# Optimization experiments

Measured on AMD Instinct MI355X. Metric: run time of the kernel, lower is better.

The kernel has to match this reference:

```python
import jax, jax.numpy as jnp
import numpy as np

N = 50000      # num nodes
E = 800000     # num edges
F = 128        # num_node_features
H = 4          # num_heads
D = 32         # output_dim (per head); H*D == F -> residual is identity
G = 8          # grid_size
K = 3          # spline order (standard KANLinear default)
NEG_SLOPE = 0.2


def _make_grid(grid_size, k):
    # uniform grid on [-1, 1], extended by k on each side: [G + 2k + 1] points
    h = 2.0 / grid_size
    return jnp.arange(-k, grid_size + k + 1, dtype=jnp.float32) * h - 1.0


def _bsplines(x, grid, k):
    # x: [N, F], grid: [G+2k+1] -> bases: [N, F, G+k] (Cox-de Boor recursion)
    xg = x[..., None]
    b = ((xg >= grid[:-1]) & (xg < grid[1:])).astype(x.dtype)
    for j in range(1, k + 1):
        left = (xg - grid[:-(j + 1)]) / (grid[j:-1] - grid[:-(j + 1)]) * b[..., :-1]
        right = (grid[j + 1:] - xg) / (grid[j + 1:] - grid[1:-j]) * b[..., 1:]
        b = left + right
    return b


def _kan_linear(x, base_w, spline_w, grid, k):
    # efficient-KAN linear, no bias: silu(x) @ Wb^T + Bspline(x) contracted with Ws
    base = jax.nn.silu(x) @ base_w.T                      # [N, O]
    bs = _bsplines(x, grid, k)                            # [N, F, G+K]
    spline = jnp.einsum('nfc,ofc->no', bs, spline_w)      # [N, O]
    return base + spline


def setup_inputs() -> dict:
    key = jax.random.key(0)
    ks = jax.random.split(key, 8)
    O = H * D
    C = G + K
    x = jax.random.normal(ks[0], (N, F), dtype=jnp.float32)
    edge_index = jax.random.randint(ks[1], (2, E), 0, N, dtype=jnp.int64)
    scale = 1.0 / np.sqrt(F)
    base_w_src = jax.random.normal(ks[2], (O, F), dtype=jnp.float32) * scale
    spline_w_src = jax.random.normal(ks[3], (O, F, C), dtype=jnp.float32) * (0.1 * scale)
    base_w_dst = jax.random.normal(ks[4], (O, F), dtype=jnp.float32) * scale
    spline_w_dst = jax.random.normal(ks[5], (O, F, C), dtype=jnp.float32) * (0.1 * scale)
    double_attn = jax.random.normal(ks[6], (1, H, D), dtype=jnp.float32) * (1.0 / np.sqrt(D))
    bias = jnp.zeros((O,), dtype=jnp.float32)
    prelu_a = jnp.asarray(0.25, dtype=jnp.float32)  # nn.PReLU default
    return {"x": x, "edge_index": edge_index,
            "base_w_src": base_w_src, "spline_w_src": spline_w_src,
            "base_w_dst": base_w_dst, "spline_w_dst": spline_w_dst,
            "double_attn": double_attn, "bias": bias, "prelu_a": prelu_a}


def reference(x, edge_index, base_w_src, spline_w_src, base_w_dst, spline_w_dst,
              double_attn, bias, prelu_a):
    grid = _make_grid(G, K)
    src = edge_index[0]
    dst = edge_index[1]
    num_nodes = x.shape[0]
    # projections (dropout is identity in eval mode)
    sp = _kan_linear(x, base_w_src, spline_w_src, grid, K).reshape(num_nodes, H, D)
    dp = _kan_linear(x, base_w_dst, spline_w_dst, grid, K).reshape(num_nodes, H, D)
    # GATv2 edge scores: leakyrelu(gather(src) + gather(dst)), then attn vector dot
    e = jax.nn.leaky_relu(sp[src] + dp[dst], NEG_SLOPE)          # [E, H, D]
    attn = jnp.sum(double_attn * e, axis=-1)                     # [E, H]
    # segment softmax over incoming edges per destination node (global max shift, as in torch)
    exp_attn = jnp.exp(attn - jnp.max(attn))                     # [E, H]
    denom = jax.ops.segment_sum(exp_attn, dst, num_segments=num_nodes)  # [Nn, H]
    alpha = exp_attn / (denom[dst] + 1e-16)                      # [E, H]
    # weighted aggregation
    msg = sp[src] * alpha[..., None]                             # [E, H, D]
    out = jax.ops.segment_sum(msg, dst, num_segments=num_nodes)  # [Nn, H, D]
    # residual: num_node_features == H*D -> identity
    out = out + x.reshape(num_nodes, H, D)
    # concat heads + bias + PReLU activation
    out = out.reshape(num_nodes, H * D) + bias
    return jnp.where(out >= 0, out, prelu_a * out)
```

## Files before the change

kernel.cpp:

```cpp
#include <hip/hip_runtime.h>
#include <math.h>

#define NN 50000
#define EE 800000
#define FF 128
#define CC 11
#define O2 256
#define KT 1536
#define NKC 8
#define AROW 200
#define NPB 768
#define NTB2 224
#define NFB 1563
#define NPACK 424
#define NTN 896
#define CAP 64

typedef __attribute__((ext_vector_type(8))) short short8;
typedef __attribute__((ext_vector_type(4))) float f32x4;
typedef unsigned int uint;
typedef unsigned short ushort;

__device__ __forceinline__ ushort bf16_rne(float v) {
  uint u = __float_as_uint(v);
  u = u + 0x7FFFu + ((u >> 16) & 1u);
  return (ushort)(u >> 16);
}
__device__ __forceinline__ float bf_lo(uint u) { return __uint_as_float(u << 16); }
__device__ __forceinline__ float bf_hi(uint u) { return __uint_as_float(u & 0xffff0000u); }

__device__ __forceinline__ void lds_barrier() {
  asm volatile("s_waitcnt lgkmcnt(0)" ::: "memory");
  __builtin_amdgcn_s_barrier();
}

__global__ __launch_bounds__(256) void repack_zero_kernel(
    const float* __restrict__ bws, const float* __restrict__ sws,
    const float* __restrict__ bwd, const float* __restrict__ swd,
    ushort* __restrict__ Wh, int* __restrict__ cur) {
  int idx = blockIdx.x * 256 + threadIdx.x;
  if (idx < NN) cur[idx] = 0;
  if (idx >= O2 * KT) return;
  int j = idx & 7;
  int lane = (idx >> 3) & 63;
  int cg = (idx >> 9) & 15;
  int g = idx >> 13;
  int col = cg * 16 + (lane & 15);
  int k = g * 32 + (lane >> 4) * 8 + j;
  int f = k / 12;
  int ch = k - f * 12;
  const float* bw = (col < 128) ? bws : bwd;
  const float* sw = (col < 128) ? sws : swd;
  int o = col & 127;
  float v = (ch == 11) ? bw[(size_t)o * FF + f] : sw[((size_t)o * FF + f) * CC + ch];
  Wh[idx] = bf16_rne(v);
}

__device__ __forceinline__ void kan_row(float xv, ushort* row) {
  row[11] = bf16_rne(xv / (1.f + __expf(-xv)));
  float u = fmaf(xv, 4.f, 7.f);
  float fj = floorf(u);
  int j = (int)fj;
  if (j >= 0 && j <= 13) {
    float tt = u - fj;
    float t2 = tt * tt, t3 = t2 * tt;
    float w0 = (1.f / 6.f) * (1.f - 3.f * tt + 3.f * t2 - t3);
    float w1 = (1.f / 6.f) * (4.f - 6.f * t2 + 3.f * t3);
    float w2 = (1.f / 6.f) * (1.f + 3.f * tt + 3.f * t2 - 3.f * t3);
    float w3 = (1.f / 6.f) * t3;
    float wv[4] = {w0, w1, w2, w3};
    int i0 = j - 3;
#pragma unroll
    for (int c = 0; c < 4; ++c) {
      int idx = i0 + c;
      if (idx >= 0 && idx <= 10) row[idx] = bf16_rne(wv[c]);
    }
  }
}

__global__ __launch_bounds__(256) void proj_fill_kernel(
    const float* __restrict__ x, const ushort* __restrict__ Wh,
    uint* __restrict__ projB, float2* __restrict__ projF,
    const int* __restrict__ ei, int* __restrict__ cur, ushort* __restrict__ scsr) {
  __shared__ ushort Ah[2][64][AROW];
  if (blockIdx.x >= NPB + NTB2) {
    int base = ((blockIdx.x - NPB - NTB2) * 256 + threadIdx.x) * 2;
    if (base + 1 < EE) {
      int2 ss = *(const int2*)(ei + base);
      int2 dd = *(const int2*)(ei + EE + base);
      int p0 = atomicAdd(&cur[dd.x], 1);
      if (p0 < CAP) scsr[(size_t)dd.x * CAP + p0] = (ushort)ss.x;
      int p1 = atomicAdd(&cur[dd.y], 1);
      if (p1 < CAP) scsr[(size_t)dd.y * CAP + p1] = (ushort)ss.y;
    } else if (base < EE) {
      int s = ei[base], d = ei[EE + base];
      int p0 = atomicAdd(&cur[d], 1);
      if (p0 < CAP) scsr[(size_t)d * CAP + p0] = (ushort)s;
    }
    return;
  }
  const int t = threadIdx.x;
  const int lane = t & 63;
  const int w = t >> 6;
  const int m = lane & 15;
  const int quad = lane >> 4;

  if (blockIdx.x >= NPB) {
    ushort(*Ath)[AROW] = Ah[0];
    const int tb = blockIdx.x - NPB;
    const int ks = tb & 7;
    const int rest = tb >> 3;
    const int tg = rest >> 1;
    const int hh = rest & 1;
    const int block0 = NPB * 64 + tg * 64;
    const int gn = block0 + lane;
    const bool valid = (gn < NN);

    {
      const float4 zero4 = make_float4(0.f, 0.f, 0.f, 0.f);
      float4 xvv = valid ? *(const float4*)(x + (size_t)gn * FF + ks * 16 + w * 4) : zero4;
      float xa[4] = {xvv.x, xvv.y, xvv.z, xvv.w};
      uint4* dz = (uint4*)&Ath[lane][w * 48];
#pragma unroll
      for (int i = 0; i < 6; ++i) dz[i] = make_uint4(0u, 0u, 0u, 0u);
#pragma unroll
      for (int jf = 0; jf < 4; ++jf) kan_row(xa[jf], &Ath[lane][w * 48 + jf * 12]);
    }

    f32x4 acc[4][2];
#pragma unroll
    for (int r = 0; r < 4; ++r)
#pragma unroll
      for (int c = 0; c < 2; ++c) acc[r][c] = (f32x4)(0.f);

    short8 bh_c[2];
#pragma unroll
    for (int c = 0; c < 2; ++c)
      bh_c[c] = *(const short8*)(Wh + (size_t)((ks * 6) * 16 + hh * 8 + w * 2 + c) * 512 +
                                 (size_t)lane * 8);
    __syncthreads();

#pragma unroll
    for (int sk = 0; sk < 6; ++sk) {
      short8 bh_n[2];
      if (sk < 5) {
#pragma unroll
        for (int c = 0; c < 2; ++c)
          bh_n[c] = *(const short8*)(Wh +
                                     (size_t)((ks * 6 + sk + 1) * 16 + hh * 8 + w * 2 + c) * 512 +
                                     (size_t)lane * 8);
      }
      short8 a0 = *(const short8*)(&Ath[0 * 16 + m][sk * 32 + quad * 8]);
      short8 a1 = *(const short8*)(&Ath[1 * 16 + m][sk * 32 + quad * 8]);
      short8 a2 = *(const short8*)(&Ath[2 * 16 + m][sk * 32 + quad * 8]);
      short8 a3 = *(const short8*)(&Ath[3 * 16 + m][sk * 32 + quad * 8]);
#pragma unroll
      for (int c = 0; c < 2; ++c) {
        acc[0][c] = __builtin_amdgcn_mfma_f32_16x16x32_bf16(a0, bh_c[c], acc[0][c], 0, 0, 0);
        acc[1][c] = __builtin_amdgcn_mfma_f32_16x16x32_bf16(a1, bh_c[c], acc[1][c], 0, 0, 0);
        acc[2][c] = __builtin_amdgcn_mfma_f32_16x16x32_bf16(a2, bh_c[c], acc[2][c], 0, 0, 0);
        acc[3][c] = __builtin_amdgcn_mfma_f32_16x16x32_bf16(a3, bh_c[c], acc[3][c], 0, 0, 0);
      }
      bh_c[0] = bh_n[0];
      bh_c[1] = bh_n[1];
    }
    const int q = hh * 4 + w;
#pragma unroll
    for (int r = 0; r < 4; ++r) {
#pragma unroll
      for (int reg = 0; reg < 4; ++reg) {
        int nl = r * 16 + quad * 4 + reg;
        projF[(size_t)(ks * NTN + tg * 64 + nl) * 128 + q * 16 + m] =
            make_float2(acc[r][0][reg], acc[r][1][reg]);
      }
    }
    return;
  }

  const int block0 = blockIdx.x * 64;
  const int gn = block0 + lane;

  auto stage = [&](float4 xvv, ushort(*buf)[AROW]) {
    float xa[4] = {xvv.x, xvv.y, xvv.z, xvv.w};
    uint4* dz = (uint4*)&buf[lane][w * 48];
#pragma unroll
    for (int i = 0; i < 6; ++i) dz[i] = make_uint4(0u, 0u, 0u, 0u);
#pragma unroll
    for (int jf = 0; jf < 4; ++jf) kan_row(xa[jf], &buf[lane][w * 48 + jf * 12]);
  };

  f32x4 acc[4][4];
#pragma unroll
  for (int r = 0; r < 4; ++r)
#pragma unroll
    for (int c = 0; c < 4; ++c) acc[r][c] = (f32x4)(0.f);

  float4 xv0 = *(const float4*)(x + (size_t)gn * FF + w * 4);
  stage(xv0, Ah[0]);
  float4 xv_next = *(const float4*)(x + (size_t)gn * FF + 16 + w * 4);

  short8 bh[2][4];
#pragma unroll
  for (int c = 0; c < 4; ++c) {
    bh[0][c] = *(const short8*)(Wh + (size_t)(0 * 16 + w * 4 + c) * 512 + (size_t)lane * 8);
    bh[1][c] = *(const short8*)(Wh + (size_t)(1 * 16 + w * 4 + c) * 512 + (size_t)lane * 8);
  }
  lds_barrier();

#pragma unroll 2
  for (int kc = 0; kc < NKC; ++kc) {
    float4 xv_pf = make_float4(0.f, 0.f, 0.f, 0.f);
    if (kc + 2 < NKC)
      xv_pf = *(const float4*)(x + (size_t)gn * FF + (kc + 2) * 16 + w * 4);
    if (kc + 1 < NKC) stage(xv_next, Ah[(kc + 1) & 1]);
#pragma unroll
    for (int sk = 0; sk < 6; ++sk) {
      const int p = sk & 1;
      short8 a0 = *(const short8*)(&Ah[kc & 1][0 * 16 + m][sk * 32 + quad * 8]);
      short8 a1 = *(const short8*)(&Ah[kc & 1][1 * 16 + m][sk * 32 + quad * 8]);
#pragma unroll
      for (int c = 0; c < 4; ++c)
        acc[0][c] = __builtin_amdgcn_mfma_f32_16x16x32_bf16(a0, bh[p][c], acc[0][c], 0, 0, 0);
#pragma unroll
      for (int c = 0; c < 4; ++c)
        acc[1][c] = __builtin_amdgcn_mfma_f32_16x16x32_bf16(a1, bh[p][c], acc[1][c], 0, 0, 0);
      short8 a2 = *(const short8*)(&Ah[kc & 1][2 * 16 + m][sk * 32 + quad * 8]);
      short8 a3 = *(const short8*)(&Ah[kc & 1][3 * 16 + m][sk * 32 + quad * 8]);
#pragma unroll
      for (int c = 0; c < 4; ++c)
        acc[2][c] = __builtin_amdgcn_mfma_f32_16x16x32_bf16(a2, bh[p][c], acc[2][c], 0, 0, 0);
#pragma unroll
      for (int c = 0; c < 4; ++c)
        acc[3][c] = __builtin_amdgcn_mfma_f32_16x16x32_bf16(a3, bh[p][c], acc[3][c], 0, 0, 0);
      int gnc = kc * 6 + sk + 2;
      if (gnc > 47) gnc = 47;
#pragma unroll
      for (int c = 0; c < 4; ++c)
        bh[p][c] = *(const short8*)(Wh + (size_t)(gnc * 16 + w * 4 + c) * 512 +
                                    (size_t)lane * 8);
    }
    lds_barrier();
    xv_next = xv_pf;
  }
#pragma unroll
  for (int r = 0; r < 4; ++r) {
#pragma unroll
    for (int reg = 0; reg < 4; ++reg) {
      int nd = block0 + r * 16 + quad * 4 + reg;
#pragma unroll
      for (int cp = 0; cp < 2; ++cp) {
        int q = 2 * w + cp;
        uint val = (uint)bf16_rne(acc[r][2 * cp][reg]) |
                   ((uint)bf16_rne(acc[r][2 * cp + 1][reg]) << 16);
        projB[(size_t)nd * 128 + q * 16 + m] = val;
      }
    }
  }
}

__global__ __launch_bounds__(256) void pack_kernel(
    const float2* __restrict__ projF, uint* __restrict__ projB) {
  int wk = blockIdx.x * 256 + threadIdx.x;
  int n = wk >> 7, p = wk & 127;
  if (n < 848) {
    float lo = 0.f, hi = 0.f;
#pragma unroll
    for (int ks = 0; ks < 8; ++ks) {
      float2 v = projF[(size_t)(ks * NTN + n) * 128 + p];
      lo += v.x;
      hi += v.y;
    }
    projB[(size_t)(NPB * 64 + n) * 128 + p] =
        (uint)bf16_rne(lo) | ((uint)bf16_rne(hi) << 16);
  }
}

__global__ __launch_bounds__(256) void aggr_kernel(
    const uint* __restrict__ projB, const ushort* __restrict__ scsr,
    const int* __restrict__ cur, const float* __restrict__ av,
    const float* __restrict__ x, const float* __restrict__ bias,
    const float* __restrict__ pa, float* __restrict__ out) {
  int d = blockIdx.x * 4 + (threadIdx.x >> 6);
  if (d >= NN) return;
  int l = threadIdx.x & 63;
  int g = l >> 4, m = l & 15;
  const uint4* pb4 = (const uint4*)projB;
  int sv = (int)scsr[(size_t)d * CAP + l];
  uint4 dpu = pb4[(size_t)d * 32 + 16 + m];
  uint du[4] = {dpu.x, dpu.y, dpu.z, dpu.w};
  float dplo[4], dphi[4], avlo[4], avhi[4];
  int cl[4];
#pragma unroll
  for (int j = 0; j < 4; ++j) {
    dplo[j] = bf_lo(du[j]);
    dphi[j] = bf_hi(du[j]);
    int p = 4 * m + j;
    cl[j] = ((p >> 4) << 5) + (p & 15);
    avlo[j] = av[cl[j]];
    avhi[j] = av[cl[j] + 16];
  }
  int cnt = cur[d];
  if (cnt > CAP) cnt = CAP;
  float acl[4] = {0.f, 0.f, 0.f, 0.f}, ach[4] = {0.f, 0.f, 0.f, 0.f};
  float den = 0.f;
  if (cnt > 0 && g < cnt) {
    const int cm = cnt - 1;
    int e1 = g + 4, e2 = g + 8;
    int s0 = __shfl(sv, g, 64);
    int s1 = __shfl(sv, e1 < cm ? e1 : cm, 64);
    int s2 = __shfl(sv, e2 < cm ? e2 : cm, 64);
    uint4 U0 = pb4[(size_t)s0 * 32 + m];
    uint4 U1 = pb4[(size_t)s1 * 32 + m];
    uint4 U2 = pb4[(size_t)s2 * 32 + m];
    for (int e = g; e < cnt; e += 4) {
      int e3 = e + 12;
      int s3 = __shfl(sv, e3 < cm ? e3 : cm, 64);
      uint4 U3 = pb4[(size_t)s3 * 32 + m];
      uint uu[4] = {U0.x, U0.y, U0.z, U0.w};
      float slo[4], shi[4];
      float vp = 0.f;
#pragma unroll
      for (int j = 0; j < 4; ++j) {
        slo[j] = bf_lo(uu[j]);
        shi[j] = bf_hi(uu[j]);
        float v0 = slo[j] + dplo[j];
        float v1 = shi[j] + dphi[j];
        v0 = (v0 >= 0.f) ? v0 : 0.2f * v0;
        v1 = (v1 >= 0.f) ? v1 : 0.2f * v1;
        vp = fmaf(v0, avlo[j], vp);
        vp = fmaf(v1, avhi[j], vp);
      }
      vp += __shfl_xor(vp, 1, 64);
      vp += __shfl_xor(vp, 2, 64);
      float e_ = __expf(vp);
#pragma unroll
      for (int j = 0; j < 4; ++j) {
        acl[j] = fmaf(e_, slo[j], acl[j]);
        ach[j] = fmaf(e_, shi[j], ach[j]);
      }
      den += e_;
      U0 = U1;
      U1 = U2;
      U2 = U3;
    }
  }
#pragma unroll
  for (int off = 16; off < 64; off <<= 1) {
    den += __shfl_xor(den, off, 64);
#pragma unroll
    for (int j = 0; j < 4; ++j) {
      acl[j] += __shfl_xor(acl[j], off, 64);
      ach[j] += __shfl_xor(ach[j], off, 64);
    }
  }
  if (g == 0) {
    float a = pa[0];
    float r = 1.f / (den + 1e-16f);
#pragma unroll
    for (int j = 0; j < 4; ++j) {
      float o0 = acl[j] * r + x[(size_t)d * FF + cl[j]] + bias[cl[j]];
      float o1 = ach[j] * r + x[(size_t)d * FF + cl[j] + 16] + bias[cl[j] + 16];
      out[(size_t)d * FF + cl[j]] = (o0 >= 0.f) ? o0 : a * o0;
      out[(size_t)d * FF + cl[j] + 16] = (o1 >= 0.f) ? o1 : a * o1;
    }
  }
}

extern "C" void kernel_launch(void* const* d_in, const int* in_sizes, int n_in,
                              void* d_out, int out_size, void* d_ws, size_t ws_size,
                              hipStream_t stream) {
  const float* x = (const float*)d_in[0];
  const int* ei = (const int*)d_in[1];
  const float* bws = (const float*)d_in[2];
  const float* sws = (const float*)d_in[3];
  const float* bwd = (const float*)d_in[4];
  const float* swd = (const float*)d_in[5];
  const float* av = (const float*)d_in[6];
  const float* bias = (const float*)d_in[7];
  const float* pa = (const float*)d_in[8];

  ushort* Wh = (ushort*)d_ws;
  uint* projB = (uint*)(Wh + (size_t)O2 * KT);
  int* cur = (int*)(projB + (size_t)NN * 128);
  ushort* scsr = (ushort*)(cur + NN);
  float2* projF = (float2*)(scsr + (size_t)NN * CAP);

  repack_zero_kernel<<<(O2 * KT + 255) / 256, 256, 0, stream>>>(bws, sws, bwd, swd, Wh, cur);
  proj_fill_kernel<<<NPB + NTB2 + NFB, 256, 0, stream>>>(x, Wh, projB, projF, ei, cur, scsr);
  pack_kernel<<<NPACK, 256, 0, stream>>>(projF, projB);
  aggr_kernel<<<(NN + 3) / 4, 256, 0, stream>>>(projB, scsr, cur, av, x, bias, pa,
                                                (float*)d_out);
}
```

Measured before the change: 216.9 us.

## Fold edge CSR fill into GEMM k-loop with pipelined atomics

Drops the separate edge-fill blocks from the projection launch. Each GEMM block now loads one edge per k-chunk, issues the slot atomic on the next chunk and writes the slot on the chunk after. This spreads the atomic and scatter latency across the MFMA work. Separately, the aggregation loop is unrolled by two and its leaky-relu becomes an fmaxf. The cost is extra registers and memory traffic inside the hot MFMA loop, which could hurt occupancy or stall the matrix pipeline.

```diff
diff --git a/kernel.cpp b/kernel.cpp
--- a/kernel.cpp
+++ b/kernel.cpp
@@ -11,7 +11,6 @@
 #define AROW 200
 #define NPB 768
 #define NTB2 224
-#define NFB 1563
 #define NPACK 424
 #define NTN 896
 #define CAP 64
@@ -83,22 +82,6 @@
     uint* __restrict__ projB, float2* __restrict__ projF,
     const int* __restrict__ ei, int* __restrict__ cur, ushort* __restrict__ scsr) {
   __shared__ ushort Ah[2][64][AROW];
-  if (blockIdx.x >= NPB + NTB2) {
-    int base = ((blockIdx.x - NPB - NTB2) * 256 + threadIdx.x) * 2;
-    if (base + 1 < EE) {
-      int2 ss = *(const int2*)(ei + base);
-      int2 dd = *(const int2*)(ei + EE + base);
-      int p0 = atomicAdd(&cur[dd.x], 1);
-      if (p0 < CAP) scsr[(size_t)dd.x * CAP + p0] = (ushort)ss.x;
-      int p1 = atomicAdd(&cur[dd.y], 1);
-      if (p1 < CAP) scsr[(size_t)dd.y * CAP + p1] = (ushort)ss.y;
-    } else if (base < EE) {
-      int s = ei[base], d = ei[EE + base];
-      int p0 = atomicAdd(&cur[d], 1);
-      if (p0 < CAP) scsr[(size_t)d * CAP + p0] = (ushort)s;
-    }
-    return;
-  }
   const int t = threadIdx.x;
   const int lane = t & 63;
   const int w = t >> 6;
@@ -205,6 +188,9 @@
     bh[0][c] = *(const short8*)(Wh + (size_t)(0 * 16 + w * 4 + c) * 512 + (size_t)lane * 8);
     bh[1][c] = *(const short8*)(Wh + (size_t)(1 * 16 + w * 4 + c) * 512 + (size_t)lane * 8);
   }
+  int ls = 0, ld = 0;
+  int as_ = 0, ad = 0, ap = 0;
+  bool lv = false, av_ = false;
   lds_barrier();
 
 #pragma unroll 2
@@ -213,6 +199,22 @@
     if (kc + 2 < NKC)
       xv_pf = *(const float4*)(x + (size_t)gn * FF + (kc + 2) * 16 + w * 4);
     if (kc + 1 < NKC) stage(xv_next, Ah[(kc + 1) & 1]);
+    if (av_) {
+      if (ap < CAP) scsr[(size_t)ad * CAP + ap] = (ushort)as_;
+      av_ = false;
+    }
+    if (lv) {
+      ap = atomicAdd(&cur[ld], 1);
+      ad = ld; as_ = ls; av_ = true; lv = false;
+    }
+    {
+      int e = (kc * NPB + (int)blockIdx.x) * 256 + t;
+      if (e < EE) {
+        ls = ei[e];
+        ld = ei[EE + e];
+        lv = true;
+      }
+    }
 #pragma unroll
     for (int sk = 0; sk < 6; ++sk) {
       const int p = sk & 1;
@@ -241,6 +243,13 @@
     }
     lds_barrier();
     xv_next = xv_pf;
+  }
+  if (av_) {
+    if (ap < CAP) scsr[(size_t)ad * CAP + ap] = (ushort)as_;
+  }
+  if (lv) {
+    int p2 = atomicAdd(&cur[ld], 1);
+    if (p2 < CAP) scsr[(size_t)ld * CAP + p2] = (ushort)ls;
   }
 #pragma unroll
   for (int r = 0; r < 4; ++r) {
@@ -312,6 +321,7 @@
     uint4 U0 = pb4[(size_t)s0 * 32 + m];
     uint4 U1 = pb4[(size_t)s1 * 32 + m];
     uint4 U2 = pb4[(size_t)s2 * 32 + m];
+#pragma unroll 2
     for (int e = g; e < cnt; e += 4) {
       int e3 = e + 12;
       int s3 = __shfl(sv, e3 < cm ? e3 : cm, 64);
@@ -325,8 +335,8 @@
         shi[j] = bf_hi(uu[j]);
         float v0 = slo[j] + dplo[j];
         float v1 = shi[j] + dphi[j];
-        v0 = (v0 >= 0.f) ? v0 : 0.2f * v0;
-        v1 = (v1 >= 0.f) ? v1 : 0.2f * v1;
+        v0 = fmaxf(v0, 0.2f * v0);
+        v1 = fmaxf(v1, 0.2f * v1);
         vp = fmaf(v0, avlo[j], vp);
         vp = fmaf(v1, avhi[j], vp);
       }
@@ -386,7 +396,7 @@
   float2* projF = (float2*)(scsr + (size_t)NN * CAP);
 
   repack_zero_kernel<<<(O2 * KT + 255) / 256, 256, 0, stream>>>(bws, sws, bwd, swd, Wh, cur);
-  proj_fill_kernel<<<NPB + NTB2 + NFB, 256, 0, stream>>>(x, Wh, projB, projF, ei, cur, scsr);
+  proj_fill_kernel<<<NPB + NTB2, 256, 0, stream>>>(x, Wh, projB, projF, ei, cur, scsr);
   pack_kernel<<<NPACK, 256, 0, stream>>>(projF, projB);
   aggr_kernel<<<(NN + 3) / 4, 256, 0, stream>>>(projB, scsr, cur, av, x, bias, pa,
                                                 (float*)d_out);
```

Result: faster. 201.9 us (-6.9%).
